# Kernel optimization log

Hardware: AMD Instinct MI355X
Metric: run time of the kernel (lower is better)

Reference implementation:

```python
import jax, jax.numpy as jnp
import numpy as np

B, N, H_DIM = 64, 128, 128
NODE_S, NODE_V = 64, 32            # irreps_node = 64x0e + 32x1o -> dim 160
OUT_S, OUT_V = 32, 16              # out irreps  = 32x0e + 16x1o -> dim 80
RBF, ZEMB, HID, LAT, EDIM, NE = 16, 32, 128, 256, 16, 512
EATT = 4096
CUTOFF = 5.0
MAXZ = 100
NODE_DIM = NODE_S + 3 * NODE_V
OUT_DIM = OUT_S + 3 * OUT_V
WN = NODE_S*OUT_S + NODE_V*OUT_S + NODE_S*OUT_V + NODE_V*OUT_V  # 4608 TP weights per edge
GATE_IN = H_DIM + H_DIM + RBF + 1

def _lin(k, fi, fo):
    return jax.random.normal(k, (fi, fo), jnp.float32) / np.sqrt(fi)

def setup_inputs() -> dict:
    ks = jax.random.split(jax.random.key(0), 24)
    flat = B * N
    att_dist = jax.random.uniform(ks[0], (EATT,), jnp.float32, 0.05, CUTOFF)
    dirs = jax.random.normal(ks[1], (EATT, 3), jnp.float32)
    dirs = dirs / jnp.linalg.norm(dirs, axis=-1, keepdims=True)
    return dict(
        h=jax.random.normal(ks[2], (B, N, H_DIM), jnp.float32),
        h_full=jax.random.normal(ks[3], (B, N, NODE_DIM), jnp.float32),
        z=jax.random.randint(ks[4], (B, N), 1, MAXZ + 1),
        mask=jnp.ones((B, N), bool),
        e_feat=jax.random.normal(ks[5], (NE, EDIM), jnp.float32),
        absorber_index=jax.random.randint(ks[6], (B,), 0, N),
        att_dst=jax.random.randint(ks[7], (EATT,), 0, flat),
        att_dist=att_dist,
        att_vec=dirs * att_dist[:, None],
        w_zemb=jax.random.normal(ks[8], (MAXZ + 1, ZEMB), jnp.float32),
        w1_rad=_lin(ks[9], ZEMB + 1 + RBF, HID), b1_rad=jnp.zeros(HID, jnp.float32),
        w2_rad=_lin(ks[10], HID, WN), b2_rad=jnp.zeros(WN, jnp.float32),
        wg1=_lin(ks[11], GATE_IN, HID), bg1=jnp.zeros(HID, jnp.float32),
        wg2=_lin(ks[12], HID, 1), bg2=jnp.zeros(1, jnp.float32),
        we1=_lin(ks[13], EDIM, HID), be1=jnp.zeros(HID, jnp.float32),
        we2=_lin(ks[14], HID, OUT_S + OUT_V), be2=jnp.ones(OUT_S + OUT_V, jnp.float32),
        wo1=_lin(ks[15], OUT_S + OUT_V, HID), bo1=jnp.zeros(HID, jnp.float32),
        wo2=_lin(ks[16], HID, HID), bo2=jnp.zeros(HID, jnp.float32),
        wo3=_lin(ks[17], HID, LAT), bo3=jnp.zeros(LAT, jnp.float32),
    )

def _core(h, h_full, z, e_feat, absorber_index, att_dst, att_dist, att_vec,
          w_zemb, w1_rad, b1_rad, w2_rad, b2_rad, wg1, bg1, wg2, bg2,
          we1, be1, we2, be2, wo1, bo1, wo2, bo2, wo3, bo3):
    B_, N_, H_ = h.shape
    flat = B_ * N_
    dt = h.dtype
    # scatter edge data into flat (B*N) buffers
    amask = jnp.zeros((flat,), bool).at[att_dst].set(True)
    dflat = jnp.zeros((flat,), dt).at[att_dst].set(att_dist.astype(dt))
    vflat = jnp.zeros((flat, 3), dt).at[att_dst].set(att_vec.astype(dt))
    eps = jnp.maximum(dflat, 1e-8)
    u = vflat / eps[:, None]
    # component-normalized real spherical harmonics, lmax=1: Y0 = 1, Y1 = sqrt(3)*u
    ys = jnp.ones((flat, 1), dt)
    yv = jnp.sqrt(jnp.asarray(3.0, dt)) * u
    # Gaussian RBF on distance
    centers = jnp.linspace(0.0, CUTOFF, RBF).astype(dt)
    width = CUTOFF / (RBF - 1)
    rbf = jnp.exp(-0.5 * ((dflat[:, None] - centers) / width) ** 2)
    zr = w_zemb[z].reshape(flat, ZEMB)
    is_abs = jax.nn.one_hot(absorber_index, N_, dtype=dt)  # (B,N)
    win = jnp.concatenate([zr, is_abs.reshape(flat, 1), rbf], -1)
    tpw = jax.nn.silu(win @ w1_rad + b1_rad) @ w2_rad + b2_rad  # (flat, WN)
    o = 0
    wA = tpw[:, o:o + NODE_S*OUT_S].reshape(flat, NODE_S, OUT_S); o += NODE_S*OUT_S
    wB = tpw[:, o:o + NODE_V*OUT_S].reshape(flat, NODE_V, OUT_S); o += NODE_V*OUT_S
    wC = tpw[:, o:o + NODE_S*OUT_V].reshape(flat, NODE_S, OUT_V); o += NODE_S*OUT_V
    wD = tpw[:, o:o + NODE_V*OUT_V].reshape(flat, NODE_V, OUT_V)
    hf = h_full.reshape(flat, NODE_DIM)
    s1 = hf[:, :NODE_S]
    v1 = hf[:, NODE_S:].reshape(flat, NODE_V, 3)
    norm = 1.0 / np.sqrt(NODE_S + NODE_V)   # TP path (fan-in) normalization
    inv_s3 = 1.0 / np.sqrt(3.0)             # CG(1,1->0) = delta/sqrt(3)
    out_s = (jnp.einsum('ei,eio->eo', s1 * ys, wA)
             + jnp.einsum('eic,ec,eio->eo', v1, yv, wB) * inv_s3) * norm
    out_v = (jnp.einsum('ei,eio->eo', s1, wC)[:, :, None] * yv[:, None, :]
             + jnp.einsum('eic,eio->eoc', v1, wD) * ys[:, :, None]) * norm
    ve = jnp.concatenate([out_s, out_v.reshape(flat, 3 * OUT_V)], -1)
    env = jnp.where(dflat < CUTOFF, 0.5 * (jnp.cos(np.pi * dflat / CUTOFF) + 1.0), 0.0)[:, None]
    ve = ve * env
    # PaiNN-style scalar edge gate
    h_abs = jnp.take_along_axis(h, absorber_index[:, None, None], axis=1)  # (B,1,H)
    gate_in = jnp.concatenate([jnp.broadcast_to(h_abs, (B_, N_, H_)), h,
                               rbf.reshape(B_, N_, RBF), is_abs[..., None]], -1)
    gate = jax.nn.sigmoid(jax.nn.silu(gate_in @ wg1 + bg1) @ wg2 + bg2).reshape(flat, 1)
    ve = ve * gate * amask[:, None].astype(dt)
    v_abs = ve.reshape(B_, N_, OUT_DIM).sum(1)  # (B, OUT_DIM)
    # energy irrep modulation: per-mul scalar from energy features
    scales = jax.nn.silu(e_feat @ we1 + be1) @ we2 + be2  # (nE, OUT_S+OUT_V)
    scale_full = jnp.concatenate([scales[:, :OUT_S], jnp.repeat(scales[:, OUT_S:], 3, axis=-1)], -1)
    v_mod = v_abs[:, None, :] * scale_full[None]  # (B, nE, OUT_DIM)
    vecs = v_mod[..., OUT_S:].reshape(B_, scales.shape[0], OUT_V, 3)
    inv = jnp.concatenate([v_mod[..., :OUT_S], jnp.sqrt(jnp.sum(vecs * vecs, -1) + 1e-12)], -1)
    x = jax.nn.silu(inv @ wo1 + bo1)
    x = jax.nn.silu(x @ wo2 + bo2)
    return x @ wo3 + bo3  # (B, nE, LAT)

def reference(h, h_full, z, mask, e_feat, absorber_index, att_dst, att_dist, att_vec,
              w_zemb, w1_rad, b1_rad, w2_rad, b2_rad, wg1, bg1, wg2, bg2,
              we1, be1, we2, be2, wo1, bo1, wo2, bo2, wo3, bo3):
    # mask is computed into att_mask in the original but never used downstream
    return _core(h, h_full, z, e_feat, absorber_index, att_dst, att_dist, att_vec,
                 w_zemb, w1_rad, b1_rad, w2_rad, b2_rad, wg1, bg1, wg2, bg2,
                 we1, be1, we2, be2, wo1, bo1, wo2, bo2, wo3, bo3)
```

## Files before the change

### kernel.cpp

```cpp
#include <hip/hip_runtime.h>
#include <math.h>

#define FLAT   8192
#define NB     64
#define OD_    80
#define NE_    512
#define EATT_  4096
#define MAXACT 4096
#define PARTW 1088

typedef __bf16 v8bf __attribute__((ext_vector_type(8)));
typedef float  v4f  __attribute__((ext_vector_type(4)));

__device__ __forceinline__ float silu_f(float x) { return x / (1.f + __expf(-x)); }
__device__ __forceinline__ float sigm_f(float x) { return 1.f / (1.f + __expf(-x)); }

__global__ void k_init(float* vabs, int* widx, int* count) {
  int t = blockIdx.x * 256 + threadIdx.x;
  if (t < FLAT) widx[t] = -1;
  if (t < NB * OD_) vabs[t] = 0.f;
  if (t == 0) *count = 0;
}

__global__ void k_scatter(const int* __restrict__ att_dst, int* widx) {
  int i = blockIdx.x * 256 + threadIdx.x;
  if (i < EATT_) atomicMax(&widx[att_dst[i]], i);
}

__global__ void k_build(const int* __restrict__ widx, int* active, int* count) {
  int j = blockIdx.x * 256 + threadIdx.x;
  if (j < FLAT && widx[j] >= 0) {
    int p = atomicAdd(count, 1);
    active[p] = j;
  }
}

__global__ void k_gabs(const int* __restrict__ abs_idx, const float* __restrict__ h,
                       const float* __restrict__ wg1, float* habs_g) {
  int b = blockIdx.x;
  int t = threadIdx.x;
  __shared__ float hs[128];
  int nabs = abs_idx[b];
  hs[t] = h[(size_t)(b * 128 + nabs) * 128 + t];
  __syncthreads();
  float g = 0.f;
  for (int c = 0; c < 128; ++c) g = fmaf(hs[c], wg1[c * 128 + t], g);
  habs_g[b * 128 + t] = g;
}

__global__ void k_wprep(const float* __restrict__ wo2, const float* __restrict__ wo3,
                        __bf16* w2h, __bf16* w2l, __bf16* w3h, __bf16* w3l) {
  int b = blockIdx.x;
  int t = threadIdx.x;
  if (b < 128) {
    float v = wo2[t * 128 + b];
    __bf16 h = (__bf16)v;
    w2h[b * 128 + t] = h;
    w2l[b * 128 + t] = (__bf16)(v - (float)h);
  } else {
    int n = b - 128;
    float v = wo3[t * 256 + n];
    __bf16 h = (__bf16)v;
    w3h[n * 128 + t] = h;
    w3l[n * 128 + t] = (__bf16)(v - (float)h);
  }
}

__global__ void k_wprep2(const float* __restrict__ w2, __bf16* wh, __bf16* wl) {
  int n = blockIdx.x * 32 + (threadIdx.x >> 3);
  int k0 = (threadIdx.x & 7) * 16;
  union { __bf16 b[16]; uint4 u[2]; } H, L;
#pragma unroll
  for (int kk = 0; kk < 16; ++kk) {
    float v = w2[(size_t)(k0 + kk) * 4608 + n];
    __bf16 hv = (__bf16)v;
    H.b[kk] = hv;
    L.b[kk] = (__bf16)(v - (float)hv);
  }
  *(uint4*)(wh + (size_t)n * 128 + k0)     = H.u[0];
  *(uint4*)(wh + (size_t)n * 128 + k0 + 8) = H.u[1];
  *(uint4*)(wl + (size_t)n * 128 + k0)     = L.u[0];
  *(uint4*)(wl + (size_t)n * 128 + k0 + 8) = L.u[1];
}

__global__ void k_node(const int* __restrict__ count, const int* __restrict__ active,
                       const int* __restrict__ widx,
                       const float* __restrict__ att_dist, const float* __restrict__ att_vec,
                       const int* __restrict__ z, const float* __restrict__ w_zemb,
                       const int* __restrict__ abs_idx,
                       const float* __restrict__ w1_rad, const float* __restrict__ b1_rad,
                       const float* __restrict__ h, const float* __restrict__ habs_g,
                       const float* __restrict__ wg1, const float* __restrict__ bg1,
                       const float* __restrict__ wg2, const float* __restrict__ bg2,
                       const float* __restrict__ h_full,
                       __bf16* ah_glob, __bf16* al_glob,
                       float* coef_glob, float* meta_f, int* meta_b) {
  int pos = blockIdx.x;
  if (pos >= *count) return;
  int t = threadIdx.x;
  __shared__ float win[49];
  __shared__ float yv_s[3];
  __shared__ float red[128];
  __shared__ float sh_d;

  int j = active[pos];
  int b = j >> 7;
  int n = j & 127;
  int e = widx[j];

  if (t == 0) {
    float d = att_dist[e];
    sh_d = d;
    float eps = fmaxf(d, 1e-8f);
    const float s3 = 1.7320508075688772f;
    yv_s[0] = s3 * att_vec[e * 3 + 0] / eps;
    yv_s[1] = s3 * att_vec[e * 3 + 1] / eps;
    yv_s[2] = s3 * att_vec[e * 3 + 2] / eps;
  }
  int nabs = abs_idx[b];
  float isab = (n == nabs) ? 1.f : 0.f;
  if (t < 32) win[t] = w_zemb[z[j] * 32 + t];
  if (t == 32) win[32] = isab;
  if (t >= 33 && t < 49) {
    int k = t - 33;
    float d = att_dist[e];
    float x = (d - (float)k * (1.f / 3.f)) * 3.f;
    win[t] = __expf(-0.5f * x * x);
  }
  __syncthreads();

  {
    float s = b1_rad[t];
    for (int k = 0; k < 49; ++k) s = fmaf(win[k], w1_rad[k * 128 + t], s);
    float av = silu_f(s);
    __bf16 hv = (__bf16)av;
    ah_glob[pos * 128 + t] = hv;
    al_glob[pos * 128 + t] = (__bf16)(av - (float)hv);
  }

  {
    float g = bg1[t] + habs_g[b * 128 + t];
    const float* hn = h + (size_t)j * 128;
    for (int c = 0; c < 128; ++c) g = fmaf(hn[c], wg1[(128 + c) * 128 + t], g);
    for (int k = 0; k < 16; ++k)  g = fmaf(win[33 + k], wg1[(256 + k) * 128 + t], g);
    g = fmaf(isab, wg1[272 * 128 + t], g);
    red[t] = silu_f(g) * wg2[t];
  }
  __syncthreads();

  const float* hf = h_full + (size_t)j * 160;
  if (t < 64) coef_glob[pos * 192 + t] = hf[t];
  if (t >= 64 && t < 96) {
    int i = t - 64;
    float pv = hf[64 + i * 3 + 0] * yv_s[0] + hf[64 + i * 3 + 1] * yv_s[1] +
               hf[64 + i * 3 + 2] * yv_s[2];
    coef_glob[pos * 192 + t] = pv * 0.5773502691896258f;
  }
  if (t < 96) coef_glob[pos * 192 + 96 + t] = hf[64 + t];

  if (t == 0) {
    float tot = 0.f;
    for (int k = 0; k < 128; ++k) tot += red[k];
    tot += bg2[0];
    float gate = sigm_f(tot);
    float d = sh_d;
    float env = (d < 5.f) ? 0.5f * (__cosf(3.14159265358979323846f * d * 0.2f) + 1.f) : 0.f;
    meta_f[pos * 4 + 0] = yv_s[0];
    meta_f[pos * 4 + 1] = yv_s[1];
    meta_f[pos * 4 + 2] = yv_s[2];
    meta_f[pos * 4 + 3] = gate * env;
    meta_b[pos] = b;
  }
}

__global__ __launch_bounds__(256) void k_mrgemm(
    const int* __restrict__ count,
    const __bf16* Ah, const __bf16* Al,
    const __bf16* __restrict__ Bh, const __bf16* __restrict__ Bl,
    const float* __restrict__ b2, const float* __restrict__ coef_glob,
    float* __restrict__ part) {
  int cc = blockIdx.x;
  int nbase = blockIdx.y * 128;
  int cnt = *count;
  if (nbase >= cnt) return;
  int t = threadIdx.x;
  int w = t >> 6, l = t & 63;
  int kg = l >> 4, ln = l & 15;
  int cbase = cc * 128;

  __shared__ v8bf Bs[2][2][8][64];

  size_t brow0 = (size_t)(cbase + w * 16 + ln) * 128 + kg * 8;
  size_t brow1 = (size_t)(cbase + (w + 4) * 16 + ln) * 128 + kg * 8;
  size_t arow0 = (size_t)(nbase + (2 * w) * 16 + ln) * 128 + kg * 8;
  size_t arow1 = (size_t)(nbase + (2 * w + 1) * 16 + ln) * 128 + kg * 8;

  v8bf rb0 = *(const v8bf*)(Bh + brow0);
  v8bf rb1 = *(const v8bf*)(Bh + brow1);
  v8bf rb2 = *(const v8bf*)(Bl + brow0);
  v8bf rb3 = *(const v8bf*)(Bl + brow1);
  v8bf ah0 = *(const v8bf*)(Ah + arow0);
  v8bf al0 = *(const v8bf*)(Al + arow0);
  v8bf ah1 = *(const v8bf*)(Ah + arow1);
  v8bf al1 = *(const v8bf*)(Al + arow1);
  Bs[0][0][w][l]     = rb0;
  Bs[0][0][w + 4][l] = rb1;
  Bs[0][1][w][l]     = rb2;
  Bs[0][1][w + 4][l] = rb3;
  __syncthreads();

  v4f acc[2][8];
  v4f z4 = {0.f, 0.f, 0.f, 0.f};
#pragma unroll
  for (int i = 0; i < 2; ++i)
#pragma unroll
    for (int j = 0; j < 8; ++j) acc[i][j] = z4;

  for (int kb = 0; kb < 4; ++kb) {
    int cur = kb & 1;
    v8bf nb0, nb1, nb2, nb3, nh0, nl0, nh1, nl1;
    if (kb < 3) {
      int off = (kb + 1) * 32;
      nb0 = *(const v8bf*)(Bh + brow0 + off);
      nb1 = *(const v8bf*)(Bh + brow1 + off);
      nb2 = *(const v8bf*)(Bl + brow0 + off);
      nb3 = *(const v8bf*)(Bl + brow1 + off);
      nh0 = *(const v8bf*)(Ah + arow0 + off);
      nl0 = *(const v8bf*)(Al + arow0 + off);
      nh1 = *(const v8bf*)(Ah + arow1 + off);
      nl1 = *(const v8bf*)(Al + arow1 + off);
    }
#pragma unroll
    for (int nt = 0; nt < 8; ++nt) {
      v8bf bh = Bs[cur][0][nt][l];
      v8bf bl = Bs[cur][1][nt][l];
      acc[0][nt] = __builtin_amdgcn_mfma_f32_16x16x32_bf16(ah0, bh, acc[0][nt], 0, 0, 0);
      acc[0][nt] = __builtin_amdgcn_mfma_f32_16x16x32_bf16(al0, bh, acc[0][nt], 0, 0, 0);
      acc[0][nt] = __builtin_amdgcn_mfma_f32_16x16x32_bf16(ah0, bl, acc[0][nt], 0, 0, 0);
      acc[1][nt] = __builtin_amdgcn_mfma_f32_16x16x32_bf16(ah1, bh, acc[1][nt], 0, 0, 0);
      acc[1][nt] = __builtin_amdgcn_mfma_f32_16x16x32_bf16(al1, bh, acc[1][nt], 0, 0, 0);
      acc[1][nt] = __builtin_amdgcn_mfma_f32_16x16x32_bf16(ah1, bl, acc[1][nt], 0, 0, 0);
    }
    if (kb < 3) {
      int nxt = cur ^ 1;
      Bs[nxt][0][w][l]     = nb0;
      Bs[nxt][0][w + 4][l] = nb1;
      Bs[nxt][1][w][l]     = nb2;
      Bs[nxt][1][w + 4][l] = nb3;
      ah0 = nh0; al0 = nl0; ah1 = nh1; al1 = nl1;
    }
    __syncthreads();
  }

  float b2v[8];
#pragma unroll
  for (int nt = 0; nt < 8; ++nt) b2v[nt] = b2[cbase + nt * 16 + ln];

#pragma unroll
  for (int mi = 0; mi < 2; ++mi) {
    int nodeb = nbase + (2 * w + mi) * 16 + kg * 4;
#pragma unroll
    for (int j = 0; j < 4; ++j) {
      int nd = nodeb + j;
      if (nd >= cnt) continue;
      const float* cf = coef_glob + (size_t)nd * 192;
      if (cc < 24) {
        float s0 = 0.f, s1 = 0.f;
#pragma unroll
        for (int m = 0; m < 4; ++m) {
          float c = cf[cc * 4 + m];
          s0 = fmaf(acc[mi][2 * m][j] + b2v[2 * m], c, s0);
          s1 = fmaf(acc[mi][2 * m + 1][j] + b2v[2 * m + 1], c, s1);
        }
        float* pp = part + (size_t)nd * PARTW + cc * 32 + ln;
        pp[0]  = s0;
        pp[16] = s1;
      } else if (cc < 32) {
        float s = 0.f;
#pragma unroll
        for (int nt = 0; nt < 8; ++nt)
          s = fmaf(acc[mi][nt][j] + b2v[nt], cf[(cc - 24) * 8 + nt], s);
        part[(size_t)nd * PARTW + 768 + (cc - 24) * 16 + ln] = s;
      } else {
        float s0 = 0.f, s1 = 0.f, s2 = 0.f;
#pragma unroll
        for (int nt = 0; nt < 8; ++nt) {
          float x = acc[mi][nt][j] + b2v[nt];
          const float* c3 = cf + 96 + ((cc - 32) * 8 + nt) * 3;
          s0 = fmaf(x, c3[0], s0);
          s1 = fmaf(x, c3[1], s1);
          s2 = fmaf(x, c3[2], s2);
        }
        float* pp = part + (size_t)nd * PARTW + 896 + (cc - 32) * 48 + ln;
        pp[0]  = s0;
        pp[16] = s1;
        pp[32] = s2;
      }
    }
  }
}

__global__ void k_combine(const int* __restrict__ count, const float* __restrict__ part,
                          const float* __restrict__ meta_f, const int* __restrict__ meta_b,
                          float* vabs) {
  int t = threadIdx.x;
  int pos = blockIdx.x * 2 + (t >> 7);
  int slot = t & 127;
  if (pos >= *count || slot >= 96) return;
  const float* pp = part + (size_t)pos * PARTW;
  float s = 0.f;
  if (slot < 32) {
#pragma unroll
    for (int c = 0; c < 24; ++c) s += pp[c * 32 + slot];
  } else if (slot < 48) {
#pragma unroll
    for (int c = 0; c < 8; ++c) s += pp[768 + c * 16 + (slot - 32)];
  } else {
#pragma unroll
    for (int c = 0; c < 4; ++c) s += pp[896 + c * 48 + (slot - 48)];
  }
  float sc = meta_f[pos * 4 + 3] * 0.10206207261596577f;
  float* vb = vabs + meta_b[pos] * 80;
  if (slot < 32) {
    unsafeAtomicAdd(&vb[slot], s * sc);
  } else if (slot < 48) {
    int o = slot - 32;
    float q = s * sc;
    unsafeAtomicAdd(&vb[32 + o * 3 + 0], q * meta_f[pos * 4 + 0]);
    unsafeAtomicAdd(&vb[32 + o * 3 + 1], q * meta_f[pos * 4 + 1]);
    unsafeAtomicAdd(&vb[32 + o * 3 + 2], q * meta_f[pos * 4 + 2]);
  } else {
    int s2 = slot - 48;
    int comp = s2 >> 4, o = s2 & 15;
    unsafeAtomicAdd(&vb[32 + o * 3 + comp], s * sc);
  }
}

__global__ void k_scales(const float* __restrict__ e_feat,
                         const float* __restrict__ we1, const float* __restrict__ be1,
                         const float* __restrict__ we2, const float* __restrict__ be2,
                         float* sfull) {
  int row = blockIdx.x;
  int t = threadIdx.x;
  __shared__ float hid[128];
  const float* ef = e_feat + row * 16;
  float s = be1[t];
  for (int k = 0; k < 16; ++k) s = fmaf(ef[k], we1[k * 128 + t], s);
  hid[t] = silu_f(s);
  __syncthreads();
  if (t < 48) {
    float o = be2[t];
    for (int k = 0; k < 128; ++k) o = fmaf(hid[k], we2[k * 48 + t], o);
    if (t < 32) sfull[row * 80 + t] = o;
    else {
      int oo = t - 32;
      sfull[row * 80 + 32 + oo * 3 + 0] = o;
      sfull[row * 80 + 32 + oo * 3 + 1] = o;
      sfull[row * 80 + 32 + oo * 3 + 2] = o;
    }
  }
}

__global__ __launch_bounds__(256) void k_hg1(const float* __restrict__ vabs,
                                             const float* __restrict__ sfull,
                                             const float* __restrict__ wo1,
                                             const float* __restrict__ bo1,
                                             __bf16* __restrict__ xh,
                                             __bf16* __restrict__ xl) {
  int rbase = blockIdx.x * 64;
  int b = rbase >> 9;
  int e0 = rbase & 511;
  int t = threadIdx.x;
  int tx = t & 15, ty = t >> 4;
  int n0 = ty * 4;

  __shared__ float w_s[48 * 128];
  __shared__ float invt[48][64];
  __shared__ float va[80];

  if (t < 80) va[t] = vabs[b * 80 + t];
  {
    const float4* wg = (const float4*)wo1;
    float4* ws4 = (float4*)w_s;
#pragma unroll
    for (int it = 0; it < 6; ++it) ws4[t + it * 256] = wg[t + it * 256];
  }
  __syncthreads();

  for (int idx = t; idx < 48 * 64; idx += 256) {
    int cd = idx >> 6, r = idx & 63;
    const float* sf = sfull + (size_t)(e0 + r) * 80;
    float v;
    if (cd < 32) v = va[cd] * sf[cd];
    else {
      int base = 32 + (cd - 32) * 3;
      float m0 = va[base + 0] * sf[base + 0];
      float m1 = va[base + 1] * sf[base + 1];
      float m2 = va[base + 2] * sf[base + 2];
      v = sqrtf(m0 * m0 + m1 * m1 + m2 * m2 + 1e-12f);
    }
    invt[cd][r] = v;
  }
  __syncthreads();

  float acc[4][8];
#pragma unroll
  for (int i = 0; i < 4; ++i)
#pragma unroll
    for (int j = 0; j < 8; ++j) acc[i][j] = 0.f;

  for (int k = 0; k < 48; ++k) {
    float4 av  = *(const float4*)&invt[k][n0];
    float4 w0  = *(const float4*)&w_s[k * 128 + tx * 4];
    float4 w1v = *(const float4*)&w_s[k * 128 + 64 + tx * 4];
#pragma unroll
    for (int i = 0; i < 4; ++i) {
      float a = (i == 0) ? av.x : (i == 1) ? av.y : (i == 2) ? av.z : av.w;
      acc[i][0] = fmaf(a, w0.x,  acc[i][0]);
      acc[i][1] = fmaf(a, w0.y,  acc[i][1]);
      acc[i][2] = fmaf(a, w0.z,  acc[i][2]);
      acc[i][3] = fmaf(a, w0.w,  acc[i][3]);
      acc[i][4] = fmaf(a, w1v.x, acc[i][4]);
      acc[i][5] = fmaf(a, w1v.y, acc[i][5]);
      acc[i][6] = fmaf(a, w1v.z, acc[i][6]);
      acc[i][7] = fmaf(a, w1v.w, acc[i][7]);
    }
  }

  float4 bq0 = *(const float4*)(bo1 + tx * 4);
  float4 bq1 = *(const float4*)(bo1 + 64 + tx * 4);
#pragma unroll
  for (int i = 0; i < 4; ++i) {
    size_t row = (size_t)(rbase + n0 + i);
    float q0[4] = {silu_f(acc[i][0] + bq0.x), silu_f(acc[i][1] + bq0.y),
                   silu_f(acc[i][2] + bq0.z), silu_f(acc[i][3] + bq0.w)};
    float q1[4] = {silu_f(acc[i][4] + bq1.x), silu_f(acc[i][5] + bq1.y),
                   silu_f(acc[i][6] + bq1.z), silu_f(acc[i][7] + bq1.w)};
    union { __bf16 bb[4]; uint2 u; } H, L;
#pragma unroll
    for (int e = 0; e < 4; ++e) {
      __bf16 hv = (__bf16)q0[e];
      H.bb[e] = hv;
      L.bb[e] = (__bf16)(q0[e] - (float)hv);
    }
    *(uint2*)(xh + row * 128 + tx * 4) = H.u;
    *(uint2*)(xl + row * 128 + tx * 4) = L.u;
#pragma unroll
    for (int e = 0; e < 4; ++e) {
      __bf16 hv = (__bf16)q1[e];
      H.bb[e] = hv;
      L.bb[e] = (__bf16)(q1[e] - (float)hv);
    }
    *(uint2*)(xh + row * 128 + 64 + tx * 4) = H.u;
    *(uint2*)(xl + row * 128 + 64 + tx * 4) = L.u;
  }
}

template<int MODE>
__global__ __launch_bounds__(256) void k_mgemm(
    const __bf16* Ah, const __bf16* Al,
    const __bf16* __restrict__ Bh, const __bf16* __restrict__ Bl,
    const float* __restrict__ bias,
    __bf16* Oh, __bf16* Ol, float* __restrict__ Of) {
  int rbase = blockIdx.y * 64;
  int cbase = blockIdx.x * 128;
  int t = threadIdx.x;
  int w = t >> 6;
  int l = t & 63;
  int kg = l >> 4, ln = l & 15;

  __shared__ v8bf As[2][2][4][64];
  __shared__ v8bf Bs[2][2][8][64];

  size_t arow  = (size_t)(rbase + w * 16 + ln) * 128 + kg * 8;
  int nt0 = w, nt1 = w + 4;
  size_t brow0 = (size_t)(cbase + nt0 * 16 + ln) * 128 + kg * 8;
  size_t brow1 = (size_t)(cbase + nt1 * 16 + ln) * 128 + kg * 8;

  v8bf ra0, ra1, rb0, rb1, rb2, rb3;
  ra0 = *(const v8bf*)(Ah + arow);
  ra1 = *(const v8bf*)(Al + arow);
  rb0 = *(const v8bf*)(Bh + brow0);
  rb1 = *(const v8bf*)(Bh + brow1);
  rb2 = *(const v8bf*)(Bl + brow0);
  rb3 = *(const v8bf*)(Bl + brow1);
  As[0][0][w][l]   = ra0;
  As[0][1][w][l]   = ra1;
  Bs[0][0][nt0][l] = rb0;
  Bs[0][0][nt1][l] = rb1;
  Bs[0][1][nt0][l] = rb2;
  Bs[0][1][nt1][l] = rb3;
  __syncthreads();

  v4f acc[8];
  v4f z4 = {0.f, 0.f, 0.f, 0.f};
#pragma unroll
  for (int i = 0; i < 8; ++i) acc[i] = z4;

  for (int kb = 0; kb < 4; ++kb) {
    int cur = kb & 1;
    if (kb < 3) {
      int off = (kb + 1) * 32;
      ra0 = *(const v8bf*)(Ah + arow + off);
      ra1 = *(const v8bf*)(Al + arow + off);
      rb0 = *(const v8bf*)(Bh + brow0 + off);
      rb1 = *(const v8bf*)(Bh + brow1 + off);
      rb2 = *(const v8bf*)(Bl + brow0 + off);
      rb3 = *(const v8bf*)(Bl + brow1 + off);
    }
    v8bf ah  = As[cur][0][w][l];
    v8bf alo = As[cur][1][w][l];
#pragma unroll
    for (int nt = 0; nt < 8; ++nt) {
      v8bf bh = Bs[cur][0][nt][l];
      v8bf bl = Bs[cur][1][nt][l];
      acc[nt] = __builtin_amdgcn_mfma_f32_16x16x32_bf16(ah,  bh, acc[nt], 0, 0, 0);
      acc[nt] = __builtin_amdgcn_mfma_f32_16x16x32_bf16(alo, bh, acc[nt], 0, 0, 0);
      acc[nt] = __builtin_amdgcn_mfma_f32_16x16x32_bf16(ah,  bl, acc[nt], 0, 0, 0);
    }
    if (kb < 3) {
      int nxt = cur ^ 1;
      As[nxt][0][w][l]   = ra0;
      As[nxt][1][w][l]   = ra1;
      Bs[nxt][0][nt0][l] = rb0;
      Bs[nxt][0][nt1][l] = rb1;
      Bs[nxt][1][nt0][l] = rb2;
      Bs[nxt][1][nt1][l] = rb3;
    }
    __syncthreads();
  }

  int r0 = rbase + w * 16 + kg * 4;
#pragma unroll
  for (int nt = 0; nt < 8; ++nt) {
    float bv = bias[cbase + nt * 16 + ln];
#pragma unroll
    for (int j = 0; j < 4; ++j) {
      float x = acc[nt][j] + bv;
      if (MODE == 0) {
        x = silu_f(x);
        __bf16 hv = (__bf16)x;
        size_t o = (size_t)(r0 + j) * 128 + nt * 16 + ln;
        Oh[o] = hv;
        Ol[o] = (__bf16)(x - (float)hv);
      } else {
        Of[(size_t)(r0 + j) * 256 + cbase + nt * 16 + ln] = x;
      }
    }
  }
}

extern "C" void kernel_launch(void* const* d_in, const int* in_sizes, int n_in,
                              void* d_out, int out_size, void* d_ws, size_t ws_size,
                              hipStream_t stream) {
  const float* h        = (const float*)d_in[0];
  const float* h_full   = (const float*)d_in[1];
  const int*   z        = (const int*)d_in[2];
  const float* e_feat   = (const float*)d_in[4];
  const int*   abs_idx  = (const int*)d_in[5];
  const int*   att_dst  = (const int*)d_in[6];
  const float* att_dist = (const float*)d_in[7];
  const float* att_vec  = (const float*)d_in[8];
  const float* w_zemb   = (const float*)d_in[9];
  const float* w1_rad   = (const float*)d_in[10];
  const float* b1_rad   = (const float*)d_in[11];
  const float* w2_rad   = (const float*)d_in[12];
  const float* b2_rad   = (const float*)d_in[13];
  const float* wg1      = (const float*)d_in[14];
  const float* bg1      = (const float*)d_in[15];
  const float* wg2      = (const float*)d_in[16];
  const float* bg2      = (const float*)d_in[17];
  const float* we1      = (const float*)d_in[18];
  const float* be1      = (const float*)d_in[19];
  const float* we2      = (const float*)d_in[20];
  const float* be2      = (const float*)d_in[21];
  const float* wo1      = (const float*)d_in[22];
  const float* bo1      = (const float*)d_in[23];
  const float* wo2      = (const float*)d_in[24];
  const float* bo2      = (const float*)d_in[25];
  const float* wo3      = (const float*)d_in[26];
  const float* bo3      = (const float*)d_in[27];
  float* out = (float*)d_out;

  float* meta_f  = (float*)d_ws;
  float* vabs    = meta_f + MAXACT * 4;
  float* sfull   = vabs + NB * OD_;
  float* habs_g  = sfull + NE_ * OD_;
  __bf16* w2t_h  = (__bf16*)(habs_g + NB * 128);
  __bf16* w2t_l  = w2t_h + 128 * 128;
  __bf16* w3t_h  = w2t_l + 128 * 128;
  __bf16* w3t_l  = w3t_h + 256 * 128;
  int* widx   = (int*)(w3t_l + 256 * 128);
  int* active = widx + FLAT;
  int* meta_b = active + MAXACT;
  int* count  = meta_b + MAXACT;
  float* big  = (float*)(count + 15);
  __bf16* ah_glob  = (__bf16*)big;
  __bf16* al_glob  = ah_glob + MAXACT * 128;
  float* coef_glob = (float*)(al_glob + MAXACT * 128);
  __bf16* w2rt_h   = (__bf16*)(coef_glob + MAXACT * 192);
  __bf16* w2rt_l   = w2rt_h + 4608 * 128;
  float* part      = (float*)(w2rt_l + 4608 * 128);
  __bf16* xh       = (__bf16*)big;
  __bf16* xl       = xh + (size_t)32768 * 128;

  k_init<<<32, 256, 0, stream>>>(vabs, widx, count);
  k_wprep<<<384, 128, 0, stream>>>(wo2, wo3, w2t_h, w2t_l, w3t_h, w3t_l);
  k_wprep2<<<144, 256, 0, stream>>>(w2_rad, w2rt_h, w2rt_l);
  k_scatter<<<16, 256, 0, stream>>>(att_dst, widx);
  k_build<<<32, 256, 0, stream>>>(widx, active, count);
  k_gabs<<<NB, 128, 0, stream>>>(abs_idx, h, wg1, habs_g);
  k_node<<<MAXACT, 128, 0, stream>>>(count, active, widx, att_dist, att_vec, z, w_zemb,
                                     abs_idx, w1_rad, b1_rad, h, habs_g, wg1, bg1, wg2, bg2,
                                     h_full, ah_glob, al_glob, coef_glob, meta_f, meta_b);
  k_mrgemm<<<dim3(36, 32), 256, 0, stream>>>(count, ah_glob, al_glob, w2rt_h, w2rt_l,
                                             b2_rad, coef_glob, part);
  k_combine<<<MAXACT / 2, 256, 0, stream>>>(count, part, meta_f, meta_b, vabs);
  k_scales<<<512, 128, 0, stream>>>(e_feat, we1, be1, we2, be2, sfull);
  k_hg1<<<512, 256, 0, stream>>>(vabs, sfull, wo1, bo1, xh, xl);
  k_mgemm<0><<<dim3(1, 512), 256, 0, stream>>>(xh, xl, w2t_h, w2t_l, bo2,
                                               xh, xl, nullptr);
  k_mgemm<1><<<dim3(2, 512), 256, 0, stream>>>(xh, xl, w3t_h, w3t_l, bo3,
                                               nullptr, nullptr, out);
}
```

Before: 248.4 us.

## Merge prep kernels, batch four nodes per block, fuse combine with scales

Folds init, the three weight transpose/split kernels and the absorber gate projection into one k_prep launch. The weight transposes now stage through a padded LDS tile so global reads are coalesced float4 loads. The node kernel processes four active nodes per block so each wg1/w1_rad weight load is reused four times, and h rows are staged in shared memory. The combine and energy-scale kernels share one launch, which cuts launch count at the cost of more divergent block roles and larger shared memory per block.

```diff
diff --git a/kernel.cpp b/kernel.cpp
--- a/kernel.cpp
+++ b/kernel.cpp
@@ -15,11 +15,69 @@
 __device__ __forceinline__ float silu_f(float x) { return x / (1.f + __expf(-x)); }
 __device__ __forceinline__ float sigm_f(float x) { return 1.f / (1.f + __expf(-x)); }
 
-__global__ void k_init(float* vabs, int* widx, int* count) {
-  int t = blockIdx.x * 256 + threadIdx.x;
-  if (t < FLAT) widx[t] = -1;
-  if (t < NB * OD_) vabs[t] = 0.f;
-  if (t == 0) *count = 0;
+__device__ __forceinline__ void transpose_split(const float* __restrict__ src, int ld,
+                                                int nbase, __bf16* wh, __bf16* wl,
+                                                float (*lds)[129]) {
+  int t = threadIdx.x;
+#pragma unroll
+  for (int it = 0; it < 16; ++it) {
+    int idx = it * 256 + t;
+    int r = idx >> 5, c4 = idx & 31;
+    float4 v = *(const float4*)(src + (size_t)r * ld + nbase + c4 * 4);
+    lds[r][c4 * 4 + 0] = v.x;
+    lds[r][c4 * 4 + 1] = v.y;
+    lds[r][c4 * 4 + 2] = v.z;
+    lds[r][c4 * 4 + 3] = v.w;
+  }
+  __syncthreads();
+  int n = t >> 1, kh = (t & 1) * 64;
+  union { __bf16 b[64]; uint4 u[8]; } H, L;
+#pragma unroll
+  for (int k = 0; k < 64; ++k) {
+    float v = lds[kh + k][n];
+    __bf16 hv = (__bf16)v;
+    H.b[k] = hv;
+    L.b[k] = (__bf16)(v - (float)hv);
+  }
+  uint4* ph = (uint4*)(wh + (size_t)(nbase + n) * 128 + kh);
+  uint4* pl = (uint4*)(wl + (size_t)(nbase + n) * 128 + kh);
+#pragma unroll
+  for (int i = 0; i < 8; ++i) { ph[i] = H.u[i]; pl[i] = L.u[i]; }
+}
+
+__global__ __launch_bounds__(256) void k_prep(
+    const float* __restrict__ w2_rad, const float* __restrict__ wo2,
+    const float* __restrict__ wo3,
+    const int* __restrict__ abs_idx, const float* __restrict__ h,
+    const float* __restrict__ wg1,
+    __bf16* w2rt_h, __bf16* w2rt_l, __bf16* w2t_h, __bf16* w2t_l,
+    __bf16* w3t_h, __bf16* w3t_l,
+    float* habs_g, float* vabs, int* widx, int* count) {
+  __shared__ float lds[128][129];
+  int bid = blockIdx.x;
+  int t = threadIdx.x;
+  if (bid < 36) {
+    transpose_split(w2_rad, 4608, bid * 128, w2rt_h, w2rt_l, lds);
+  } else if (bid < 37) {
+    transpose_split(wo2, 128, 0, w2t_h, w2t_l, lds);
+  } else if (bid < 39) {
+    transpose_split(wo3, 256, (bid - 37) * 128, w3t_h, w3t_l, lds);
+  } else if (bid < 71) {
+    float* hs = &lds[0][0];
+    int half = t >> 7, tt = t & 127;
+    int b = (bid - 39) * 2 + half;
+    int nabs = abs_idx[b];
+    hs[half * 128 + tt] = h[(size_t)(b * 128 + nabs) * 128 + tt];
+    __syncthreads();
+    float g = 0.f;
+    for (int c = 0; c < 128; ++c) g = fmaf(hs[half * 128 + c], wg1[c * 128 + tt], g);
+    habs_g[b * 128 + tt] = g;
+  } else {
+    int g = (bid - 71) * 256 + t;
+    if (g < FLAT) widx[g] = -1;
+    if (g < NB * OD_) vabs[g] = 0.f;
+    if (g == 0) *count = 0;
+  }
 }
 
 __global__ void k_scatter(const int* __restrict__ att_dst, int* widx) {
@@ -35,141 +93,145 @@
   }
 }
 
-__global__ void k_gabs(const int* __restrict__ abs_idx, const float* __restrict__ h,
-                       const float* __restrict__ wg1, float* habs_g) {
-  int b = blockIdx.x;
+__global__ __launch_bounds__(128) void k_node4(
+    const int* __restrict__ count, const int* __restrict__ active,
+    const int* __restrict__ widx,
+    const float* __restrict__ att_dist, const float* __restrict__ att_vec,
+    const int* __restrict__ z, const float* __restrict__ w_zemb,
+    const int* __restrict__ abs_idx,
+    const float* __restrict__ w1_rad, const float* __restrict__ b1_rad,
+    const float* __restrict__ h, const float* __restrict__ habs_g,
+    const float* __restrict__ wg1, const float* __restrict__ bg1,
+    const float* __restrict__ wg2, const float* __restrict__ bg2,
+    const float* __restrict__ h_full,
+    __bf16* ah_glob, __bf16* al_glob,
+    float* coef_glob, float* meta_f, int* meta_b) {
+  int cnt = *count;
+  int pbase = blockIdx.x * 4;
+  if (pbase >= cnt) return;
   int t = threadIdx.x;
-  __shared__ float hs[128];
-  int nabs = abs_idx[b];
-  hs[t] = h[(size_t)(b * 128 + nabs) * 128 + t];
-  __syncthreads();
-  float g = 0.f;
-  for (int c = 0; c < 128; ++c) g = fmaf(hs[c], wg1[c * 128 + t], g);
-  habs_g[b * 128 + t] = g;
-}
-
-__global__ void k_wprep(const float* __restrict__ wo2, const float* __restrict__ wo3,
-                        __bf16* w2h, __bf16* w2l, __bf16* w3h, __bf16* w3l) {
-  int b = blockIdx.x;
-  int t = threadIdx.x;
-  if (b < 128) {
-    float v = wo2[t * 128 + b];
-    __bf16 h = (__bf16)v;
-    w2h[b * 128 + t] = h;
-    w2l[b * 128 + t] = (__bf16)(v - (float)h);
-  } else {
-    int n = b - 128;
-    float v = wo3[t * 256 + n];
-    __bf16 h = (__bf16)v;
-    w3h[n * 128 + t] = h;
-    w3l[n * 128 + t] = (__bf16)(v - (float)h);
-  }
-}
-
-__global__ void k_wprep2(const float* __restrict__ w2, __bf16* wh, __bf16* wl) {
-  int n = blockIdx.x * 32 + (threadIdx.x >> 3);
-  int k0 = (threadIdx.x & 7) * 16;
-  union { __bf16 b[16]; uint4 u[2]; } H, L;
-#pragma unroll
-  for (int kk = 0; kk < 16; ++kk) {
-    float v = w2[(size_t)(k0 + kk) * 4608 + n];
-    __bf16 hv = (__bf16)v;
-    H.b[kk] = hv;
-    L.b[kk] = (__bf16)(v - (float)hv);
-  }
-  *(uint4*)(wh + (size_t)n * 128 + k0)     = H.u[0];
-  *(uint4*)(wh + (size_t)n * 128 + k0 + 8) = H.u[1];
-  *(uint4*)(wl + (size_t)n * 128 + k0)     = L.u[0];
-  *(uint4*)(wl + (size_t)n * 128 + k0 + 8) = L.u[1];
-}
-
-__global__ void k_node(const int* __restrict__ count, const int* __restrict__ active,
-                       const int* __restrict__ widx,
-                       const float* __restrict__ att_dist, const float* __restrict__ att_vec,
-                       const int* __restrict__ z, const float* __restrict__ w_zemb,
-                       const int* __restrict__ abs_idx,
-                       const float* __restrict__ w1_rad, const float* __restrict__ b1_rad,
-                       const float* __restrict__ h, const float* __restrict__ habs_g,
-                       const float* __restrict__ wg1, const float* __restrict__ bg1,
-                       const float* __restrict__ wg2, const float* __restrict__ bg2,
-                       const float* __restrict__ h_full,
-                       __bf16* ah_glob, __bf16* al_glob,
-                       float* coef_glob, float* meta_f, int* meta_b) {
-  int pos = blockIdx.x;
-  if (pos >= *count) return;
-  int t = threadIdx.x;
-  __shared__ float win[49];
-  __shared__ float yv_s[3];
-  __shared__ float red[128];
-  __shared__ float sh_d;
-
-  int j = active[pos];
-  int b = j >> 7;
-  int n = j & 127;
-  int e = widx[j];
-
-  if (t == 0) {
-    float d = att_dist[e];
-    sh_d = d;
+
+  __shared__ float win[4][49];
+  __shared__ float yv_s[4][3];
+  __shared__ float sh_d[4];
+  __shared__ float red[4][128];
+  __shared__ float hsh[4][128];
+
+  bool ok[4];
+  int jj[4], ee[4], bb[4];
+  float isab[4];
+#pragma unroll
+  for (int q = 0; q < 4; ++q) {
+    int pos = pbase + q;
+    ok[q] = pos < cnt;
+    jj[q] = ok[q] ? active[pos] : 0;
+    ee[q] = ok[q] ? widx[jj[q]] : 0;
+    if (ee[q] < 0) ee[q] = 0;
+    bb[q] = jj[q] >> 7;
+    isab[q] = ((jj[q] & 127) == abs_idx[bb[q]]) ? 1.f : 0.f;
+  }
+
+  if (t < 4) {
+    int q = t;
+    float d = att_dist[ee[q]];
+    sh_d[q] = d;
     float eps = fmaxf(d, 1e-8f);
     const float s3 = 1.7320508075688772f;
-    yv_s[0] = s3 * att_vec[e * 3 + 0] / eps;
-    yv_s[1] = s3 * att_vec[e * 3 + 1] / eps;
-    yv_s[2] = s3 * att_vec[e * 3 + 2] / eps;
-  }
-  int nabs = abs_idx[b];
-  float isab = (n == nabs) ? 1.f : 0.f;
-  if (t < 32) win[t] = w_zemb[z[j] * 32 + t];
-  if (t == 32) win[32] = isab;
-  if (t >= 33 && t < 49) {
-    int k = t - 33;
-    float d = att_dist[e];
-    float x = (d - (float)k * (1.f / 3.f)) * 3.f;
-    win[t] = __expf(-0.5f * x * x);
+    yv_s[q][0] = s3 * att_vec[ee[q] * 3 + 0] / eps;
+    yv_s[q][1] = s3 * att_vec[ee[q] * 3 + 1] / eps;
+    yv_s[q][2] = s3 * att_vec[ee[q] * 3 + 2] / eps;
+  }
+#pragma unroll
+  for (int q = 0; q < 4; ++q) {
+    if (t < 32) win[q][t] = w_zemb[z[jj[q]] * 32 + t];
+    if (t == 32) win[q][32] = isab[q];
+    if (t >= 33 && t < 49) {
+      int k = t - 33;
+      float d = att_dist[ee[q]];
+      float x = (d - (float)k * (1.f / 3.f)) * 3.f;
+      win[q][t] = __expf(-0.5f * x * x);
+    }
+    hsh[q][t] = h[(size_t)jj[q] * 128 + t];
   }
   __syncthreads();
 
   {
-    float s = b1_rad[t];
-    for (int k = 0; k < 49; ++k) s = fmaf(win[k], w1_rad[k * 128 + t], s);
-    float av = silu_f(s);
-    __bf16 hv = (__bf16)av;
-    ah_glob[pos * 128 + t] = hv;
-    al_glob[pos * 128 + t] = (__bf16)(av - (float)hv);
+    float s[4];
+    float bv = b1_rad[t];
+#pragma unroll
+    for (int q = 0; q < 4; ++q) s[q] = bv;
+    for (int k = 0; k < 49; ++k) {
+      float wv = w1_rad[k * 128 + t];
+#pragma unroll
+      for (int q = 0; q < 4; ++q) s[q] = fmaf(win[q][k], wv, s[q]);
+    }
+#pragma unroll
+    for (int q = 0; q < 4; ++q) {
+      if (ok[q]) {
+        float av = silu_f(s[q]);
+        __bf16 hv = (__bf16)av;
+        ah_glob[(size_t)(pbase + q) * 128 + t] = hv;
+        al_glob[(size_t)(pbase + q) * 128 + t] = (__bf16)(av - (float)hv);
+      }
+    }
   }
 
   {
-    float g = bg1[t] + habs_g[b * 128 + t];
-    const float* hn = h + (size_t)j * 128;
-    for (int c = 0; c < 128; ++c) g = fmaf(hn[c], wg1[(128 + c) * 128 + t], g);
-    for (int k = 0; k < 16; ++k)  g = fmaf(win[33 + k], wg1[(256 + k) * 128 + t], g);
-    g = fmaf(isab, wg1[272 * 128 + t], g);
-    red[t] = silu_f(g) * wg2[t];
+    float g[4];
+#pragma unroll
+    for (int q = 0; q < 4; ++q) g[q] = bg1[t] + habs_g[bb[q] * 128 + t];
+    for (int c = 0; c < 128; ++c) {
+      float wv = wg1[(128 + c) * 128 + t];
+#pragma unroll
+      for (int q = 0; q < 4; ++q) g[q] = fmaf(hsh[q][c], wv, g[q]);
+    }
+    for (int k = 0; k < 16; ++k) {
+      float wv = wg1[(256 + k) * 128 + t];
+#pragma unroll
+      for (int q = 0; q < 4; ++q) g[q] = fmaf(win[q][33 + k], wv, g[q]);
+    }
+    {
+      float wv = wg1[272 * 128 + t];
+#pragma unroll
+      for (int q = 0; q < 4; ++q) g[q] = fmaf(isab[q], wv, g[q]);
+    }
+    float w2v = wg2[t];
+#pragma unroll
+    for (int q = 0; q < 4; ++q) red[q][t] = silu_f(g[q]) * w2v;
   }
   __syncthreads();
 
-  const float* hf = h_full + (size_t)j * 160;
-  if (t < 64) coef_glob[pos * 192 + t] = hf[t];
-  if (t >= 64 && t < 96) {
-    int i = t - 64;
-    float pv = hf[64 + i * 3 + 0] * yv_s[0] + hf[64 + i * 3 + 1] * yv_s[1] +
-               hf[64 + i * 3 + 2] * yv_s[2];
-    coef_glob[pos * 192 + t] = pv * 0.5773502691896258f;
-  }
-  if (t < 96) coef_glob[pos * 192 + 96 + t] = hf[64 + t];
-
-  if (t == 0) {
-    float tot = 0.f;
-    for (int k = 0; k < 128; ++k) tot += red[k];
-    tot += bg2[0];
-    float gate = sigm_f(tot);
-    float d = sh_d;
-    float env = (d < 5.f) ? 0.5f * (__cosf(3.14159265358979323846f * d * 0.2f) + 1.f) : 0.f;
-    meta_f[pos * 4 + 0] = yv_s[0];
-    meta_f[pos * 4 + 1] = yv_s[1];
-    meta_f[pos * 4 + 2] = yv_s[2];
-    meta_f[pos * 4 + 3] = gate * env;
-    meta_b[pos] = b;
+#pragma unroll
+  for (int q = 0; q < 4; ++q) {
+    if (!ok[q]) continue;
+    int pos = pbase + q;
+    const float* hf = h_full + (size_t)jj[q] * 160;
+    if (t < 64) coef_glob[pos * 192 + t] = hf[t];
+    if (t >= 64 && t < 96) {
+      int i = t - 64;
+      float pv = hf[64 + i * 3 + 0] * yv_s[q][0] + hf[64 + i * 3 + 1] * yv_s[q][1] +
+                 hf[64 + i * 3 + 2] * yv_s[q][2];
+      coef_glob[pos * 192 + t] = pv * 0.5773502691896258f;
+    }
+    if (t < 96) coef_glob[pos * 192 + 96 + t] = hf[64 + t];
+  }
+
+  if (t < 4) {
+    int q = t;
+    if (ok[q]) {
+      int pos = pbase + q;
+      float tot = 0.f;
+      for (int k = 0; k < 128; ++k) tot += red[q][k];
+      tot += bg2[0];
+      float gate = sigm_f(tot);
+      float d = sh_d[q];
+      float env = (d < 5.f) ? 0.5f * (__cosf(3.14159265358979323846f * d * 0.2f) + 1.f) : 0.f;
+      meta_f[pos * 4 + 0] = yv_s[q][0];
+      meta_f[pos * 4 + 1] = yv_s[q][1];
+      meta_f[pos * 4 + 2] = yv_s[q][2];
+      meta_f[pos * 4 + 3] = gate * env;
+      meta_b[pos] = bb[q];
+    }
   }
 }
 
@@ -300,63 +362,64 @@
   }
 }
 
-__global__ void k_combine(const int* __restrict__ count, const float* __restrict__ part,
-                          const float* __restrict__ meta_f, const int* __restrict__ meta_b,
-                          float* vabs) {
+__global__ __launch_bounds__(256) void k_post(
+    const int* __restrict__ count, const float* __restrict__ part,
+    const float* __restrict__ meta_f, const int* __restrict__ meta_b, float* vabs,
+    const float* __restrict__ e_feat,
+    const float* __restrict__ we1, const float* __restrict__ be1,
+    const float* __restrict__ we2, const float* __restrict__ be2, float* sfull) {
+  __shared__ float hid[128];
   int t = threadIdx.x;
-  int pos = blockIdx.x * 2 + (t >> 7);
-  int slot = t & 127;
-  if (pos >= *count || slot >= 96) return;
-  const float* pp = part + (size_t)pos * PARTW;
-  float s = 0.f;
-  if (slot < 32) {
-#pragma unroll
-    for (int c = 0; c < 24; ++c) s += pp[c * 32 + slot];
-  } else if (slot < 48) {
-#pragma unroll
-    for (int c = 0; c < 8; ++c) s += pp[768 + c * 16 + (slot - 32)];
+  if (blockIdx.x < 2048) {
+    int pos = blockIdx.x * 2 + (t >> 7);
+    int slot = t & 127;
+    if (pos >= *count || slot >= 96) return;
+    const float* pp = part + (size_t)pos * PARTW;
+    float s = 0.f;
+    if (slot < 32) {
+#pragma unroll
+      for (int c = 0; c < 24; ++c) s += pp[c * 32 + slot];
+    } else if (slot < 48) {
+#pragma unroll
+      for (int c = 0; c < 8; ++c) s += pp[768 + c * 16 + (slot - 32)];
+    } else {
+#pragma unroll
+      for (int c = 0; c < 4; ++c) s += pp[896 + c * 48 + (slot - 48)];
+    }
+    float sc = meta_f[pos * 4 + 3] * 0.10206207261596577f;
+    float* vb = vabs + meta_b[pos] * 80;
+    if (slot < 32) {
+      unsafeAtomicAdd(&vb[slot], s * sc);
+    } else if (slot < 48) {
+      int o = slot - 32;
+      float q = s * sc;
+      unsafeAtomicAdd(&vb[32 + o * 3 + 0], q * meta_f[pos * 4 + 0]);
+      unsafeAtomicAdd(&vb[32 + o * 3 + 1], q * meta_f[pos * 4 + 1]);
+      unsafeAtomicAdd(&vb[32 + o * 3 + 2], q * meta_f[pos * 4 + 2]);
+    } else {
+      int s2 = slot - 48;
+      int comp = s2 >> 4, o = s2 & 15;
+      unsafeAtomicAdd(&vb[32 + o * 3 + comp], s * sc);
+    }
   } else {
-#pragma unroll
-    for (int c = 0; c < 4; ++c) s += pp[896 + c * 48 + (slot - 48)];
-  }
-  float sc = meta_f[pos * 4 + 3] * 0.10206207261596577f;
-  float* vb = vabs + meta_b[pos] * 80;
-  if (slot < 32) {
-    unsafeAtomicAdd(&vb[slot], s * sc);
-  } else if (slot < 48) {
-    int o = slot - 32;
-    float q = s * sc;
-    unsafeAtomicAdd(&vb[32 + o * 3 + 0], q * meta_f[pos * 4 + 0]);
-    unsafeAtomicAdd(&vb[32 + o * 3 + 1], q * meta_f[pos * 4 + 1]);
-    unsafeAtomicAdd(&vb[32 + o * 3 + 2], q * meta_f[pos * 4 + 2]);
-  } else {
-    int s2 = slot - 48;
-    int comp = s2 >> 4, o = s2 & 15;
-    unsafeAtomicAdd(&vb[32 + o * 3 + comp], s * sc);
-  }
-}
-
-__global__ void k_scales(const float* __restrict__ e_feat,
-                         const float* __restrict__ we1, const float* __restrict__ be1,
-                         const float* __restrict__ we2, const float* __restrict__ be2,
-                         float* sfull) {
-  int row = blockIdx.x;
-  int t = threadIdx.x;
-  __shared__ float hid[128];
-  const float* ef = e_feat + row * 16;
-  float s = be1[t];
-  for (int k = 0; k < 16; ++k) s = fmaf(ef[k], we1[k * 128 + t], s);
-  hid[t] = silu_f(s);
-  __syncthreads();
-  if (t < 48) {
-    float o = be2[t];
-    for (int k = 0; k < 128; ++k) o = fmaf(hid[k], we2[k * 48 + t], o);
-    if (t < 32) sfull[row * 80 + t] = o;
-    else {
-      int oo = t - 32;
-      sfull[row * 80 + 32 + oo * 3 + 0] = o;
-      sfull[row * 80 + 32 + oo * 3 + 1] = o;
-      sfull[row * 80 + 32 + oo * 3 + 2] = o;
+    int row = blockIdx.x - 2048;
+    if (t < 128) {
+      const float* ef = e_feat + row * 16;
+      float s = be1[t];
+      for (int k = 0; k < 16; ++k) s = fmaf(ef[k], we1[k * 128 + t], s);
+      hid[t] = silu_f(s);
+    }
+    __syncthreads();
+    if (t < 48) {
+      float o = be2[t];
+      for (int k = 0; k < 128; ++k) o = fmaf(hid[k], we2[k * 48 + t], o);
+      if (t < 32) sfull[row * 80 + t] = o;
+      else {
+        int oo = t - 32;
+        sfull[row * 80 + 32 + oo * 3 + 0] = o;
+        sfull[row * 80 + 32 + oo * 3 + 1] = o;
+        sfull[row * 80 + 32 + oo * 3 + 2] = o;
+      }
     }
   }
 }
@@ -604,19 +667,18 @@
   __bf16* xh       = (__bf16*)big;
   __bf16* xl       = xh + (size_t)32768 * 128;
 
-  k_init<<<32, 256, 0, stream>>>(vabs, widx, count);
-  k_wprep<<<384, 128, 0, stream>>>(wo2, wo3, w2t_h, w2t_l, w3t_h, w3t_l);
-  k_wprep2<<<144, 256, 0, stream>>>(w2_rad, w2rt_h, w2rt_l);
+  k_prep<<<103, 256, 0, stream>>>(w2_rad, wo2, wo3, abs_idx, h, wg1,
+                                  w2rt_h, w2rt_l, w2t_h, w2t_l, w3t_h, w3t_l,
+                                  habs_g, vabs, widx, count);
   k_scatter<<<16, 256, 0, stream>>>(att_dst, widx);
   k_build<<<32, 256, 0, stream>>>(widx, active, count);
-  k_gabs<<<NB, 128, 0, stream>>>(abs_idx, h, wg1, habs_g);
-  k_node<<<MAXACT, 128, 0, stream>>>(count, active, widx, att_dist, att_vec, z, w_zemb,
-                                     abs_idx, w1_rad, b1_rad, h, habs_g, wg1, bg1, wg2, bg2,
-                                     h_full, ah_glob, al_glob, coef_glob, meta_f, meta_b);
+  k_node4<<<1024, 128, 0, stream>>>(count, active, widx, att_dist, att_vec, z, w_zemb,
+                                    abs_idx, w1_rad, b1_rad, h, habs_g, wg1, bg1, wg2, bg2,
+                                    h_full, ah_glob, al_glob, coef_glob, meta_f, meta_b);
   k_mrgemm<<<dim3(36, 32), 256, 0, stream>>>(count, ah_glob, al_glob, w2rt_h, w2rt_l,
                                              b2_rad, coef_glob, part);
-  k_combine<<<MAXACT / 2, 256, 0, stream>>>(count, part, meta_f, meta_b, vabs);
-  k_scales<<<512, 128, 0, stream>>>(e_feat, we1, be1, we2, be2, sfull);
+  k_post<<<2560, 256, 0, stream>>>(count, part, meta_f, meta_b, vabs,
+                                   e_feat, we1, be1, we2, be2, sfull);
   k_hg1<<<512, 256, 0, stream>>>(vabs, sfull, wo1, bo1, xh, xl);
   k_mgemm<0><<<dim3(1, 512), 256, 0, stream>>>(xh, xl, w2t_h, w2t_l, bo2,
                                                xh, xl, nullptr);
```

After: 234.5 us. 5.6% less time.
